# Kernel optimization log

Measured on AMD Instinct MI355X. Metric: run time of the kernel, lower is better.

## Reference

```python
import jax, jax.numpy as jnp
import numpy as np

BN_EPS = 1e-5


def _bn_relu(h, gamma, beta):
    # BatchNorm1d in training mode: normalize over (batch, length) per channel
    mean = h.mean(axis=(0, 2), keepdims=True)
    var = h.var(axis=(0, 2), keepdims=True)
    h = (h - mean) * jax.lax.rsqrt(var + BN_EPS)
    h = h * gamma[None, :, None] + beta[None, :, None]
    return jax.nn.relu(h)


def _gather(ldesc, idx):
    # ldesc: [B, D, N], idx: [B, M] -> [B, D, M]
    B, D, N = ldesc.shape
    M = idx.shape[1]
    return jnp.take_along_axis(ldesc, jnp.broadcast_to(idx[:, None, :], (B, D, M)), axis=2)


def _scatter_mean(src, idx, N):
    # per-batch scatter-mean: src [B, D, M], idx [B, M] -> [B, D, N]
    def one(s, i):
        D = s.shape[0]
        sums = jnp.zeros((D, N), s.dtype).at[:, i].add(s)
        cnts = jnp.zeros((N,), s.dtype).at[i].add(1.0)
        return sums / jnp.maximum(cnts, 1.0)[None, :]
    return jax.vmap(one)(src, idx)


def _endpoint_update(ldesc, line_enc, idx, W1, b1, g1, bt1, W2, b2):
    B, D, _ = ldesc.shape
    ld = _gather(ldesc, idx)                                   # [B, D, 2L]
    # flip endpoint pairs: neighbor endpoint of each endpoint
    neigh = ld.reshape(B, D, -1, 2)[..., ::-1].reshape(B, D, -1)
    msg = jnp.concatenate([ld, neigh, line_enc], axis=1)       # [B, 3D, 2L]
    h = jnp.einsum('oc,bcm->bom', W1, msg) + b1[None, :, None]  # Conv1d k=1
    h = _bn_relu(h, g1, bt1)
    out = jnp.einsum('oc,bcm->bom', W2, h) + b2[None, :, None]
    return out                                                  # [B, D, 2L]


def setup_inputs() -> dict:
    key = jax.random.key(0)
    ks = jax.random.split(key, 12)
    B, D, N, M = 8, 256, 8192, 8192
    inp = {
        'ldesc0': jax.random.normal(ks[0], (B, D, N), jnp.float32),
        'ldesc1': jax.random.normal(ks[1], (B, D, N), jnp.float32),
        'line_enc0': jax.random.normal(ks[2], (B, D, M), jnp.float32),
        'line_enc1': jax.random.normal(ks[3], (B, D, M), jnp.float32),
        'lines_junc_idx0': jax.random.randint(ks[4], (B, M), 0, N),
        'lines_junc_idx1': jax.random.randint(ks[5], (B, M), 0, N),
        'W1': jax.random.normal(ks[6], (2 * D, 3 * D), jnp.float32) * (1.0 / np.sqrt(3 * D)),
        'b1': jnp.zeros((2 * D,), jnp.float32),
        'g1': jnp.ones((2 * D,), jnp.float32),
        'bt1': jnp.zeros((2 * D,), jnp.float32),
        'W2': jax.random.normal(ks[7], (D, 2 * D), jnp.float32) * (1.0 / np.sqrt(2 * D)),
        'b2': jnp.zeros((D,), jnp.float32),
    }
    return inp


def reference(ldesc0, ldesc1, line_enc0, line_enc1, lines_junc_idx0, lines_junc_idx1,
              W1, b1, g1, bt1, W2, b2):
    N = ldesc0.shape[2]
    up0 = _endpoint_update(ldesc0, line_enc0, lines_junc_idx0, W1, b1, g1, bt1, W2, b2)
    up1 = _endpoint_update(ldesc1, line_enc1, lines_junc_idx1, W1, b1, g1, bt1, W2, b2)
    out0 = ldesc0 + _scatter_mean(up0, lines_junc_idx0, N)
    out1 = ldesc1 + _scatter_mean(up1, lines_junc_idx1, N)
    return (out0, out1)
```

## Files before the change

kernel.cpp:

```cpp
#include <hip/hip_runtime.h>
#include <hip/hip_bf16.h>

#define B_  8
#define D_  256
#define N_  8192
#define M_  8192
#define O1_ 512
#define K1_ 768
#define K2_ 512

typedef unsigned short u16;
typedef __attribute__((ext_vector_type(8))) short bf8;
typedef __attribute__((ext_vector_type(4))) float f4;

static __device__ __forceinline__ float bf2f(u16 u) {
    unsigned v = ((unsigned)u) << 16;
    return __uint_as_float(v);
}
static __device__ __forceinline__ u16 f2bf(float f) {
    __hip_bfloat16 h = __float2bfloat16(f);
    return *reinterpret_cast<u16*>(&h);
}
static __device__ __forceinline__ void gl_lds16(const u16* g, u16* l) {
    __builtin_amdgcn_global_load_lds((const __attribute__((address_space(1))) void*)g,
                                     (__attribute__((address_space(3))) void*)l, 16, 0, 0);
}
static __device__ __forceinline__ int swz64(int r) {
    return (((r >> 1) & 1) << 4) | (((r >> 2) & 1) << 5);
}

__global__ __launch_bounds__(256) void k_transpose_bf16(const float* __restrict__ src,
                                                        u16* __restrict__ dst, int R, int C) {
    __shared__ float t[32][33];
    const int b  = blockIdx.z;
    const int c0 = blockIdx.x * 32, r0 = blockIdx.y * 32;
    const int tx = threadIdx.x, ty = threadIdx.y;
    const float* s = src + (size_t)b * R * C;
    u16* d = dst + (size_t)b * C * R;
#pragma unroll
    for (int i = 0; i < 4; ++i) {
        int r = r0 + ty + i * 8;
        t[ty + i * 8][tx] = s[(size_t)r * C + (c0 + tx)];
    }
    __syncthreads();
#pragma unroll
    for (int i = 0; i < 4; ++i) {
        int c = c0 + ty + i * 8;
        d[(size_t)c * R + (r0 + tx)] = f2bf(t[tx][ty + i * 8]);
    }
}

__global__ __launch_bounds__(256) void k_convert_w(const float* __restrict__ W1, const float* __restrict__ W2,
                                                   u16* __restrict__ W1b, u16* __restrict__ W2b) {
    int i = blockIdx.x * 256 + threadIdx.x;
    const int n1 = O1_ * K1_;
    const int n2 = D_ * K2_;
    if (i < n1) W1b[i] = f2bf(W1[i]);
    int j = i - n1;
    if (j >= 0 && j < n2) W2b[j] = f2bf(W2[j]);
}

#define NT1 24
__global__ __launch_bounds__(512, 2) void k_gemm1(const u16* __restrict__ W1b,
                                                  const u16* __restrict__ Tld,
                                                  const u16* __restrict__ Tle,
                                                  const int* __restrict__ idx,
                                                  u16* __restrict__ hbuf) {
    __shared__ u16 LA[4][256 * 32];
    __shared__ u16 LB[4][256 * 32];
    const int b  = blockIdx.z;
    const int o0 = blockIdx.y * 256;
    const int m0 = blockIdx.x * 256;
    const int tid = threadIdx.x;
    const int w = tid >> 6, l = tid & 63;
    const int wr = w >> 2;
    const int wcn = w & 3;

    const int srow   = tid >> 2;
    const int scol16 = (tid & 3) * 16;

    int na[2], nb[2], mrow[2];
    const u16* aSrc[2];
    int bcol[2];
#pragma unroll
    for (int j = 0; j < 2; ++j) {
        int r = srow + j * 128;
        int m = m0 + r;
        mrow[j] = m;
        na[j] = idx[b * M_ + m];
        nb[j] = idx[b * M_ + (m ^ 1)];
        int sw = swz64(r);
        aSrc[j] = W1b + (size_t)(o0 + r) * K1_ + ((scol16 ^ sw) >> 1);
        bcol[j] = (scol16 ^ sw) >> 1;
    }

    int ar[8], br[4];
#pragma unroll
    for (int i = 0; i < 8; ++i) {
        int r = wr * 128 + i * 16 + (l & 15);
        ar[i] = r * 32 + ((((l >> 4) * 16) ^ swz64(r)) >> 1);
    }
#pragma unroll
    for (int j = 0; j < 4; ++j) {
        int r = wcn * 64 + j * 16 + (l & 15);
        br[j] = r * 32 + ((((l >> 4) * 16) ^ swz64(r)) >> 1);
    }

#define STAGE1(kt, buf)                                                              \
    {                                                                                \
        const int seg = (kt) >> 3;                                                   \
        const int off = ((kt) & 7) * 32;                                             \
        _Pragma("unroll")                                                            \
        for (int j = 0; j < 2; ++j)                                                  \
            gl_lds16(aSrc[j] + (kt) * 32, &LA[buf][j * 4096 + tid * 8]);             \
        _Pragma("unroll")                                                            \
        for (int j = 0; j < 2; ++j) {                                                \
            const u16* s;                                                            \
            if (seg == 0)      s = Tld + (size_t)(b * N_ + na[j]) * D_ + off + bcol[j]; \
            else if (seg == 1) s = Tld + (size_t)(b * N_ + nb[j]) * D_ + off + bcol[j]; \
            else               s = Tle + (size_t)(b * M_ + mrow[j]) * D_ + off + bcol[j]; \
            gl_lds16(s, &LB[buf][j * 4096 + tid * 8]);                               \
        }                                                                            \
    }

    f4 acc[8][4];
#pragma unroll
    for (int i = 0; i < 8; ++i)
#pragma unroll
        for (int j = 0; j < 4; ++j) acc[i][j] = {0.f, 0.f, 0.f, 0.f};

    STAGE1(0, 0);
    STAGE1(1, 1);
    STAGE1(2, 2);
    asm volatile("s_waitcnt vmcnt(8)" ::: "memory");
    __builtin_amdgcn_s_barrier();
    __builtin_amdgcn_sched_barrier(0);

    for (int t = 0; t < NT1; ++t) {
        const int buf = t & 3;
        if (t + 3 < NT1) STAGE1(t + 3, (t + 3) & 3);

        bf8 aF[8], bF[4];
#pragma unroll
        for (int i = 0; i < 8; ++i) aF[i] = *reinterpret_cast<const bf8*>(&LA[buf][ar[i]]);
#pragma unroll
        for (int j = 0; j < 4; ++j) bF[j] = *reinterpret_cast<const bf8*>(&LB[buf][br[j]]);

        __builtin_amdgcn_s_setprio(1);
#pragma unroll
        for (int i = 0; i < 8; ++i)
#pragma unroll
            for (int j = 0; j < 4; ++j)
                acc[i][j] = __builtin_amdgcn_mfma_f32_16x16x32_bf16(aF[i], bF[j], acc[i][j], 0, 0, 0);
        __builtin_amdgcn_s_setprio(0);

        if (t <= NT1 - 4)      asm volatile("s_waitcnt vmcnt(8)" ::: "memory");
        else if (t == NT1 - 3) asm volatile("s_waitcnt vmcnt(4)" ::: "memory");
        else                   asm volatile("s_waitcnt vmcnt(0)" ::: "memory");
        __builtin_amdgcn_s_barrier();
        __builtin_amdgcn_sched_barrier(0);
    }
#undef STAGE1

#pragma unroll
    for (int j = 0; j < 4; ++j) {
        int m = m0 + wcn * 64 + j * 16 + (l & 15);
        size_t rowbase = (size_t)(b * M_ + m) * O1_;
#pragma unroll
        for (int i = 0; i < 8; ++i) {
            int orow = o0 + wr * 128 + i * 16 + (l >> 4) * 4;
            ushort4 pk;
            pk.x = f2bf(acc[i][j].x);
            pk.y = f2bf(acc[i][j].y);
            pk.z = f2bf(acc[i][j].z);
            pk.w = f2bf(acc[i][j].w);
            *reinterpret_cast<ushort4*>(&hbuf[rowbase + orow]) = pk;
        }
    }
}

__global__ __launch_bounds__(256) void k_stats(const u16* __restrict__ hbuf, float* __restrict__ stats) {
    const int t = threadIdx.x;
    const size_t row0 = (size_t)blockIdx.x * 256;
    float s0 = 0.f, q0 = 0.f, s1 = 0.f, q1 = 0.f;
    for (int r = 0; r < 256; ++r) {
        const u16* p = hbuf + (row0 + r) * O1_;
        float v0 = bf2f(p[t]);
        float v1 = bf2f(p[t + 256]);
        s0 += v0; q0 += v0 * v0;
        s1 += v1; q1 += v1 * v1;
    }
    atomicAdd(&stats[t], s0);
    atomicAdd(&stats[O1_ + t], q0);
    atomicAdd(&stats[t + 256], s1);
    atomicAdd(&stats[O1_ + t + 256], q1);
}

__global__ void k_finalize_ac(const float* __restrict__ stats, const float* __restrict__ g1,
                              const float* __restrict__ bt1, float* __restrict__ ac) {
    int o = blockIdx.x * 256 + threadIdx.x;
    if (o >= O1_) return;
    const float inv = 1.0f / ((float)B_ * (float)M_);
    float mean = stats[o] * inv;
    float var  = stats[O1_ + o] * inv - mean * mean;
    var = fmaxf(var, 0.0f);
    float a = g1[o] * rsqrtf(var + 1e-5f);
    ac[o] = a;
    ac[O1_ + o] = bt1[o] - mean * a;
}

__global__ void k_count_int(const int* __restrict__ idx, int* __restrict__ cnt) {
    int i = blockIdx.x * 256 + threadIdx.x;
    if (i < B_ * M_) atomicAdd(&cnt[(i >> 13) * N_ + idx[i]], 1);
}

__global__ __launch_bounds__(1024) void k_scan(const int* __restrict__ cnt, int* __restrict__ offs,
                                               int* __restrict__ fill) {
    __shared__ int wsum[1024];
    const int b = blockIdx.x;
    const int t = threadIdx.x;
    const int base = b * N_;
    int v[8]; int s = 0;
#pragma unroll
    for (int k = 0; k < 8; ++k) { v[k] = cnt[base + t * 8 + k]; s += v[k]; }
    wsum[t] = s;
    __syncthreads();
    for (int off = 1; off < 1024; off <<= 1) {
        int add = (t >= off) ? wsum[t - off] : 0;
        __syncthreads();
        wsum[t] += add;
        __syncthreads();
    }
    int run = (t > 0) ? wsum[t - 1] : 0;
#pragma unroll
    for (int k = 0; k < 8; ++k) {
        offs[base + t * 8 + k] = run;
        fill[base + t * 8 + k] = run;
        run += v[k];
    }
}

__global__ void k_fill(const int* __restrict__ idx, int* __restrict__ fill, int* __restrict__ mlist) {
    int i = blockIdx.x * 256 + threadIdx.x;
    if (i < B_ * M_) {
        int b = i >> 13, m = i & (M_ - 1);
        int pos = atomicAdd(&fill[b * N_ + idx[i]], 1);
        mlist[(size_t)b * M_ + pos] = m;
    }
}

__global__ __launch_bounds__(256) void k_gemm2(const u16* __restrict__ W2b,
                                               const u16* __restrict__ hbuf,
                                               const float* __restrict__ ac,
                                               const float* __restrict__ b2,
                                               u16* __restrict__ up) {
    __shared__ u16 At[128 * 32];
    __shared__ u16 Bt[128 * 32];
    __shared__ float acs[1024];
    const int b  = blockIdx.z;
    const int d0 = blockIdx.y * 128;
    const int m0 = blockIdx.x * 128;
    const int tid = threadIdx.x;
    const int w = tid >> 6, l = tid & 63;
    const int lr = l >> 2, lc = (l & 3) * 8;

    acs[tid]       = ac[tid];
    acs[tid + 256] = ac[tid + 256];
    acs[tid + 512] = ac[tid + 512];
    acs[tid + 768] = ac[tid + 768];

    const u16* pA[2]; const u16* pB[2];
#pragma unroll
    for (int t = 0; t < 2; ++t) {
        int row = t * 64 + w * 16 + lr;
        pA[t] = W2b + (size_t)(d0 + row) * K2_ + lc;
        int m  = m0 + row;
        pB[t] = hbuf + (size_t)(b * M_ + m) * O1_ + lc;
    }
    const int wr = w >> 1, wc = w & 1;
    f4 acc[4][4];
#pragma unroll
    for (int i = 0; i < 4; ++i)
#pragma unroll
        for (int j = 0; j < 4; ++j) acc[i][j] = {0.f, 0.f, 0.f, 0.f};

    const int aoff = (wr * 64 + (l & 15)) * 32 + (l >> 4) * 8;
    const int boff = (wc * 64 + (l & 15)) * 32 + (l >> 4) * 8;
    const int bdst = (w * 16 + lr) * 32 + lc;

    __syncthreads();

    for (int kk = 0; kk < 16; ++kk) {
        const int o = kk * 32 + lc;
        f4 A0 = *reinterpret_cast<const f4*>(&acs[o]);
        f4 A1 = *reinterpret_cast<const f4*>(&acs[o + 4]);
        f4 C0 = *reinterpret_cast<const f4*>(&acs[512 + o]);
        f4 C1 = *reinterpret_cast<const f4*>(&acs[512 + o + 4]);
#pragma unroll
        for (int t = 0; t < 2; ++t) {
            gl_lds16(pA[t] + kk * 32, At + (t * 64 + w * 16) * 32);
            const ushort4* ps = reinterpret_cast<const ushort4*>(pB[t] + kk * 32);
            ushort4 v0 = ps[0], v1 = ps[1];
            union { ushort4 u4[2]; bf8 v8; } pk;
            pk.u4[0].x = f2bf(fmaxf(bf2f(v0.x) * A0.x + C0.x, 0.0f));
            pk.u4[0].y = f2bf(fmaxf(bf2f(v0.y) * A0.y + C0.y, 0.0f));
            pk.u4[0].z = f2bf(fmaxf(bf2f(v0.z) * A0.z + C0.z, 0.0f));
            pk.u4[0].w = f2bf(fmaxf(bf2f(v0.w) * A0.w + C0.w, 0.0f));
            pk.u4[1].x = f2bf(fmaxf(bf2f(v1.x) * A1.x + C1.x, 0.0f));
            pk.u4[1].y = f2bf(fmaxf(bf2f(v1.y) * A1.y + C1.y, 0.0f));
            pk.u4[1].z = f2bf(fmaxf(bf2f(v1.z) * A1.z + C1.z, 0.0f));
            pk.u4[1].w = f2bf(fmaxf(bf2f(v1.w) * A1.w + C1.w, 0.0f));
            *reinterpret_cast<bf8*>(&Bt[t * 64 * 32 + bdst]) = pk.v8;
        }
        __syncthreads();
        bf8 aF[4], bF[4];
#pragma unroll
        for (int i = 0; i < 4; ++i) aF[i] = *reinterpret_cast<const bf8*>(&At[aoff + i * 16 * 32]);
#pragma unroll
        for (int j = 0; j < 4; ++j) bF[j] = *reinterpret_cast<const bf8*>(&Bt[boff + j * 16 * 32]);
#pragma unroll
        for (int i = 0; i < 4; ++i)
#pragma unroll
            for (int j = 0; j < 4; ++j)
                acc[i][j] = __builtin_amdgcn_mfma_f32_16x16x32_bf16(aF[i], bF[j], acc[i][j], 0, 0, 0);
        __syncthreads();
    }

#pragma unroll
    for (int j = 0; j < 4; ++j) {
        int m = m0 + wc * 64 + j * 16 + (l & 15);
        size_t rowbase = (size_t)(b * M_ + m) * D_;
#pragma unroll
        for (int i = 0; i < 4; ++i) {
            int d = d0 + wr * 64 + i * 16 + (l >> 4) * 4;
            ushort4 pk;
            pk.x = f2bf(acc[i][j].x + b2[d + 0]);
            pk.y = f2bf(acc[i][j].y + b2[d + 1]);
            pk.z = f2bf(acc[i][j].z + b2[d + 2]);
            pk.w = f2bf(acc[i][j].w + b2[d + 3]);
            *reinterpret_cast<ushort4*>(&up[rowbase + d]) = pk;
        }
    }
}

__global__ __launch_bounds__(256) void k_reduce_finalize(const float* __restrict__ ldesc,
                                                         const u16* __restrict__ up,
                                                         const int* __restrict__ cnt,
                                                         const int* __restrict__ offs,
                                                         const int* __restrict__ mlist,
                                                         float* __restrict__ out) {
    __shared__ float lds[32][257];
    const int b  = blockIdx.z;
    const int n0 = blockIdx.x * 32;
    const int tx = threadIdx.x, ty = threadIdx.y;
#pragma unroll
    for (int i = 0; i < 4; ++i) {
        int nl = ty + i * 8;
        int n  = n0 + nl;
        int c   = cnt[b * N_ + n];
        int off = offs[b * N_ + n];
        float inv = 1.0f / (float)max(c, 1);
        float acc[8] = {0.f, 0.f, 0.f, 0.f, 0.f, 0.f, 0.f, 0.f};
        for (int e = 0; e < c; ++e) {
            int m = mlist[(size_t)b * M_ + off + e];
            const ushort4* row = reinterpret_cast<const ushort4*>(up + (size_t)(b * M_ + m) * D_ + tx * 8);
            ushort4 aa = row[0], bb = row[1];
            acc[0] += bf2f(aa.x); acc[1] += bf2f(aa.y); acc[2] += bf2f(aa.z); acc[3] += bf2f(aa.w);
            acc[4] += bf2f(bb.x); acc[5] += bf2f(bb.y); acc[6] += bf2f(bb.z); acc[7] += bf2f(bb.w);
        }
#pragma unroll
        for (int k = 0; k < 8; ++k) lds[nl][tx * 8 + k] = acc[k] * inv;
    }
    __syncthreads();
#pragma unroll
    for (int i = 0; i < 32; ++i) {
        int d = ty + i * 8;
        size_t o2 = (size_t)(b * D_ + d) * N_ + n0 + tx;
        out[o2] = ldesc[o2] + lds[tx][d];
    }
}

__global__ void k_marker(float* out, float v) { out[0] = v; }

extern "C" void kernel_launch(void* const* d_in, const int* in_sizes, int n_in,
                              void* d_out, int out_size, void* d_ws, size_t ws_size,
                              hipStream_t stream) {
    const float* ldesc0 = (const float*)d_in[0];
    const float* ldesc1 = (const float*)d_in[1];
    const float* le0    = (const float*)d_in[2];
    const float* le1    = (const float*)d_in[3];
    const int*   idx0   = (const int*)d_in[4];
    const int*   idx1   = (const int*)d_in[5];
    const float* W1     = (const float*)d_in[6];
    const float* g1     = (const float*)d_in[8];
    const float* bt1    = (const float*)d_in[9];
    const float* W2     = (const float*)d_in[10];
    const float* b2     = (const float*)d_in[11];
    float* out = (float*)d_out;

    char* ws = (char*)d_ws;
    const size_t oTld   = 0;
    const size_t oTle   = 33554432;
    const size_t oH     = 67108864;
    const size_t oW1b   = 134217728;
    const size_t oW2b   = oW1b + 786432;
    const size_t oStats = oW2b + 262144;
    const size_t oAC    = oStats + 4096;
    const size_t NEED   = oAC + 4096;
    if (ws_size < NEED) {
        k_marker<<<1, 1, 0, stream>>>(out, 1000.0f + (float)(ws_size >> 20));
        return;
    }
    u16*   Tld   = (u16*)(ws + oTld);
    u16*   up    = (u16*)(ws + oTld);
    u16*   Tle   = (u16*)(ws + oTle);
    int*   cnt   = (int*)(ws + oTle);
    int*   offs  = (int*)(ws + oTle + 262144);
    int*   fill  = (int*)(ws + oTle + 524288);
    int*   mlist = (int*)(ws + oTle + 786432);
    u16*   hbuf  = (u16*)(ws + oH);
    u16*   W1b   = (u16*)(ws + oW1b);
    u16*   W2b   = (u16*)(ws + oW2b);
    float* stats = (float*)(ws + oStats);
    float* ac    = (float*)(ws + oAC);

    k_convert_w<<<2048, 256, 0, stream>>>(W1, W2, W1b, W2b);

    const dim3 tb(32, 8);
    for (int s = 0; s < 2; ++s) {
        const float* ld  = s ? ldesc1 : ldesc0;
        const float* le  = s ? le1 : le0;
        const int*   idx = s ? idx1 : idx0;
        float* outp = out + (size_t)s * B_ * D_ * N_;

        k_transpose_bf16<<<dim3(N_ / 32, D_ / 32, B_), tb, 0, stream>>>(ld, Tld, D_, N_);
        k_transpose_bf16<<<dim3(M_ / 32, D_ / 32, B_), tb, 0, stream>>>(le, Tle, D_, M_);
        k_gemm1<<<dim3(M_ / 256, O1_ / 256, B_), 512, 0, stream>>>(W1b, Tld, Tle, idx, hbuf);
        hipMemsetAsync(stats, 0, 4096, stream);
        k_stats<<<256, 256, 0, stream>>>(hbuf, stats);
        k_finalize_ac<<<2, 256, 0, stream>>>(stats, g1, bt1, ac);
        hipMemsetAsync(cnt, 0, (size_t)B_ * N_ * 4, stream);
        k_count_int<<<B_ * M_ / 256, 256, 0, stream>>>(idx, cnt);
        k_scan<<<B_, 1024, 0, stream>>>(cnt, offs, fill);
        k_fill<<<B_ * M_ / 256, 256, 0, stream>>>(idx, fill, mlist);
        k_gemm2<<<dim3(M_ / 128, D_ / 128, B_), 256, 0, stream>>>(W2b, hbuf, ac, b2, up);
        k_reduce_finalize<<<dim3(N_ / 32, 1, B_), tb, 0, stream>>>(ld, up, cnt, offs, mlist, outp);
    }
}
```

Measured before the change: 485.0 us.

## Restructure gemm1 main loop into 8-wave ping-pong with split K-halves

Replaces the 4-stage LDS ring with a 2-buffer layout where each buffer holds two 32-wide K slices, and processes 64 K per iteration. Each iteration is split into four quarter phases that interleave LDS fragment reads, global-to-LDS prefetch of the next slices, and MFMA clusters, separated by barriers. The aim is finer interleaving of memory issue with matrix math and lower register pressure from holding only four A fragments at a time. The cost is many more barriers per iteration and a shallower prefetch distance, which could expose gather latency.

```diff
diff --git a/kernel.cpp b/kernel.cpp
--- a/kernel.cpp
+++ b/kernel.cpp
@@ -60,66 +60,69 @@
     if (j >= 0 && j < n2) W2b[j] = f2bf(W2[j]);
 }
 
-#define NT1 24
+#define NT1 12
 __global__ __launch_bounds__(512, 2) void k_gemm1(const u16* __restrict__ W1b,
                                                   const u16* __restrict__ Tld,
                                                   const u16* __restrict__ Tle,
                                                   const int* __restrict__ idx,
                                                   u16* __restrict__ hbuf) {
-    __shared__ u16 LA[4][256 * 32];
-    __shared__ u16 LB[4][256 * 32];
+    __shared__ u16 LA[2][2][256][32];
+    __shared__ u16 LB[2][2][256][32];
     const int b  = blockIdx.z;
     const int o0 = blockIdx.y * 256;
     const int m0 = blockIdx.x * 256;
     const int tid = threadIdx.x;
     const int w = tid >> 6, l = tid & 63;
     const int wr = w >> 2;
-    const int wcn = w & 3;
+    const int wc = w & 3;
 
     const int srow   = tid >> 2;
-    const int scol16 = (tid & 3) * 16;
-
-    int na[2], nb[2], mrow[2];
-    const u16* aSrc[2];
-    int bcol[2];
+    const int schunk = (tid & 3) * 16;
+
+    int na[2], nb[2], mm[2];
+    const u16* aS[2];
+    int bcolu[2];
 #pragma unroll
     for (int j = 0; j < 2; ++j) {
-        int r = srow + j * 128;
+        int r = j * 128 + srow;
         int m = m0 + r;
-        mrow[j] = m;
+        mm[j] = m;
         na[j] = idx[b * M_ + m];
         nb[j] = idx[b * M_ + (m ^ 1)];
-        int sw = swz64(r);
-        aSrc[j] = W1b + (size_t)(o0 + r) * K1_ + ((scol16 ^ sw) >> 1);
-        bcol[j] = (scol16 ^ sw) >> 1;
-    }
-
-    int ar[8], br[4];
+        int swu = (schunk ^ swz64(r)) >> 1;
+        aS[j]   = W1b + (size_t)(o0 + r) * K1_ + swu;
+        bcolu[j] = swu;
+    }
+
+    int aOff[8], bOff[4];
 #pragma unroll
     for (int i = 0; i < 8; ++i) {
         int r = wr * 128 + i * 16 + (l & 15);
-        ar[i] = r * 32 + ((((l >> 4) * 16) ^ swz64(r)) >> 1);
+        aOff[i] = r * 32 + ((((l >> 4) * 16) ^ swz64(r)) >> 1);
     }
 #pragma unroll
     for (int j = 0; j < 4; ++j) {
-        int r = wcn * 64 + j * 16 + (l & 15);
-        br[j] = r * 32 + ((((l >> 4) * 16) ^ swz64(r)) >> 1);
-    }
-
-#define STAGE1(kt, buf)                                                              \
+        int r = wc * 64 + j * 16 + (l & 15);
+        bOff[j] = r * 32 + ((((l >> 4) * 16) ^ swz64(r)) >> 1);
+    }
+
+#define STAGE_A1(kt, ks, buf)                                                        \
     {                                                                                \
-        const int seg = (kt) >> 3;                                                   \
-        const int off = ((kt) & 7) * 32;                                             \
         _Pragma("unroll")                                                            \
         for (int j = 0; j < 2; ++j)                                                  \
-            gl_lds16(aSrc[j] + (kt) * 32, &LA[buf][j * 4096 + tid * 8]);             \
+            gl_lds16(aS[j] + (kt) * 64 + (ks) * 32, &LA[buf][ks][j * 128][0] + tid * 8); \
+    }
+#define STAGE_B1(kt, ks, buf)                                                        \
+    {                                                                                \
+        const int seg = (kt) >> 2;                                                   \
+        const int cb  = ((kt) & 3) * 64 + (ks) * 32;                                 \
         _Pragma("unroll")                                                            \
         for (int j = 0; j < 2; ++j) {                                                \
             const u16* s;                                                            \
-            if (seg == 0)      s = Tld + (size_t)(b * N_ + na[j]) * D_ + off + bcol[j]; \
-            else if (seg == 1) s = Tld + (size_t)(b * N_ + nb[j]) * D_ + off + bcol[j]; \
-            else               s = Tle + (size_t)(b * M_ + mrow[j]) * D_ + off + bcol[j]; \
-            gl_lds16(s, &LB[buf][j * 4096 + tid * 8]);                               \
+            if (seg == 0)      s = Tld + (size_t)(b * N_ + na[j]) * D_ + cb + bcolu[j]; \
+            else if (seg == 1) s = Tld + (size_t)(b * N_ + nb[j]) * D_ + cb + bcolu[j]; \
+            else               s = Tle + (size_t)(b * M_ + mm[j]) * D_ + cb + bcolu[j]; \
+            gl_lds16(s, &LB[buf][ks][j * 128][0] + tid * 8);                         \
         }                                                                            \
     }
 
@@ -129,42 +132,99 @@
 #pragma unroll
         for (int j = 0; j < 4; ++j) acc[i][j] = {0.f, 0.f, 0.f, 0.f};
 
-    STAGE1(0, 0);
-    STAGE1(1, 1);
-    STAGE1(2, 2);
+    STAGE_A1(0, 0, 0); STAGE_B1(0, 0, 0);
+    STAGE_A1(0, 1, 0); STAGE_B1(0, 1, 0);
+    STAGE_A1(1, 0, 1); STAGE_B1(1, 0, 1);
     asm volatile("s_waitcnt vmcnt(8)" ::: "memory");
     __builtin_amdgcn_s_barrier();
     __builtin_amdgcn_sched_barrier(0);
 
     for (int t = 0; t < NT1; ++t) {
-        const int buf = t & 3;
-        if (t + 3 < NT1) STAGE1(t + 3, (t + 3) & 3);
-
-        bf8 aF[8], bF[4];
-#pragma unroll
-        for (int i = 0; i < 8; ++i) aF[i] = *reinterpret_cast<const bf8*>(&LA[buf][ar[i]]);
-#pragma unroll
-        for (int j = 0; j < 4; ++j) bF[j] = *reinterpret_cast<const bf8*>(&LB[buf][br[j]]);
-
+        const int bufp = t & 1, nbuf = bufp ^ 1;
+        const u16* baseA0 = &LA[bufp][0][0][0];
+        const u16* baseA1 = &LA[bufp][1][0][0];
+        const u16* baseB0 = &LB[bufp][0][0][0];
+        const u16* baseB1 = &LB[bufp][1][0][0];
+        bf8 aF[4], bF[4];
+
+#pragma unroll
+        for (int j = 0; j < 4; ++j) bF[j] = *reinterpret_cast<const bf8*>(baseB0 + bOff[j]);
+#pragma unroll
+        for (int ii = 0; ii < 4; ++ii) aF[ii] = *reinterpret_cast<const bf8*>(baseA0 + aOff[ii]);
+        if (t + 1 < NT1) STAGE_A1(t + 1, 1, nbuf);
+        __builtin_amdgcn_s_barrier();
+        asm volatile("s_waitcnt lgkmcnt(0)" ::: "memory");
+        __builtin_amdgcn_sched_barrier(0);
         __builtin_amdgcn_s_setprio(1);
 #pragma unroll
-        for (int i = 0; i < 8; ++i)
+        for (int ii = 0; ii < 4; ++ii)
 #pragma unroll
             for (int j = 0; j < 4; ++j)
-                acc[i][j] = __builtin_amdgcn_mfma_f32_16x16x32_bf16(aF[i], bF[j], acc[i][j], 0, 0, 0);
+                acc[ii][j] = __builtin_amdgcn_mfma_f32_16x16x32_bf16(aF[ii], bF[j], acc[ii][j], 0, 0, 0);
         __builtin_amdgcn_s_setprio(0);
-
-        if (t <= NT1 - 4)      asm volatile("s_waitcnt vmcnt(8)" ::: "memory");
-        else if (t == NT1 - 3) asm volatile("s_waitcnt vmcnt(4)" ::: "memory");
-        else                   asm volatile("s_waitcnt vmcnt(0)" ::: "memory");
-        __builtin_amdgcn_s_barrier();
-        __builtin_amdgcn_sched_barrier(0);
-    }
-#undef STAGE1
+        __builtin_amdgcn_s_barrier();
+        __builtin_amdgcn_sched_barrier(0);
+
+#pragma unroll
+        for (int ii = 0; ii < 4; ++ii) aF[ii] = *reinterpret_cast<const bf8*>(baseA0 + aOff[4 + ii]);
+        if (t + 1 < NT1) STAGE_B1(t + 1, 1, nbuf);
+        __builtin_amdgcn_s_barrier();
+        asm volatile("s_waitcnt lgkmcnt(0)" ::: "memory");
+        __builtin_amdgcn_sched_barrier(0);
+        __builtin_amdgcn_s_setprio(1);
+#pragma unroll
+        for (int ii = 0; ii < 4; ++ii)
+#pragma unroll
+            for (int j = 0; j < 4; ++j)
+                acc[4 + ii][j] = __builtin_amdgcn_mfma_f32_16x16x32_bf16(aF[ii], bF[j], acc[4 + ii][j], 0, 0, 0);
+        __builtin_amdgcn_s_setprio(0);
+        if (t < NT1 - 2) asm volatile("s_waitcnt vmcnt(8)" ::: "memory");
+        else             asm volatile("s_waitcnt vmcnt(0)" ::: "memory");
+        __builtin_amdgcn_s_barrier();
+        __builtin_amdgcn_sched_barrier(0);
+
+#pragma unroll
+        for (int j = 0; j < 4; ++j) bF[j] = *reinterpret_cast<const bf8*>(baseB1 + bOff[j]);
+#pragma unroll
+        for (int ii = 0; ii < 4; ++ii) aF[ii] = *reinterpret_cast<const bf8*>(baseA1 + aOff[ii]);
+        if (t + 2 < NT1) STAGE_A1(t + 2, 0, bufp);
+        __builtin_amdgcn_s_barrier();
+        asm volatile("s_waitcnt lgkmcnt(0)" ::: "memory");
+        __builtin_amdgcn_sched_barrier(0);
+        __builtin_amdgcn_s_setprio(1);
+#pragma unroll
+        for (int ii = 0; ii < 4; ++ii)
+#pragma unroll
+            for (int j = 0; j < 4; ++j)
+                acc[ii][j] = __builtin_amdgcn_mfma_f32_16x16x32_bf16(aF[ii], bF[j], acc[ii][j], 0, 0, 0);
+        __builtin_amdgcn_s_setprio(0);
+        __builtin_amdgcn_s_barrier();
+        __builtin_amdgcn_sched_barrier(0);
+
+#pragma unroll
+        for (int ii = 0; ii < 4; ++ii) aF[ii] = *reinterpret_cast<const bf8*>(baseA1 + aOff[4 + ii]);
+        if (t + 2 < NT1) STAGE_B1(t + 2, 0, bufp);
+        __builtin_amdgcn_s_barrier();
+        asm volatile("s_waitcnt lgkmcnt(0)" ::: "memory");
+        __builtin_amdgcn_sched_barrier(0);
+        __builtin_amdgcn_s_setprio(1);
+#pragma unroll
+        for (int ii = 0; ii < 4; ++ii)
+#pragma unroll
+            for (int j = 0; j < 4; ++j)
+                acc[4 + ii][j] = __builtin_amdgcn_mfma_f32_16x16x32_bf16(aF[ii], bF[j], acc[4 + ii][j], 0, 0, 0);
+        __builtin_amdgcn_s_setprio(0);
+        if (t < NT1 - 2) asm volatile("s_waitcnt vmcnt(8)" ::: "memory");
+        else             asm volatile("s_waitcnt vmcnt(0)" ::: "memory");
+        __builtin_amdgcn_s_barrier();
+        __builtin_amdgcn_sched_barrier(0);
+    }
+#undef STAGE_A1
+#undef STAGE_B1
 
 #pragma unroll
     for (int j = 0; j < 4; ++j) {
-        int m = m0 + wcn * 64 + j * 16 + (l & 15);
+        int m = m0 + wc * 64 + j * 16 + (l & 15);
         size_t rowbase = (size_t)(b * M_ + m) * O1_;
 #pragma unroll
         for (int i = 0; i < 8; ++i) {
```

Measured after the change: 453.4 us. 1.07x faster.
